# Kernel optimization log

Measured on AMD Instinct MI355X. Metric: run time of the kernel, lower is better.

## Reference

```python
import jax, jax.numpy as jnp
import numpy as np

EPS_ENERGY = 1e-05
EPS_NORM = 1e-05
DN = ('NWC', 'WIO', 'NWC')  # conv1d dimension numbers: (B,L,C) x (K,Cin,Cout)


def setup_inputs() -> dict:
    key = jax.random.key(0)
    k1, k2 = jax.random.split(key)
    B, L, C = 16, 32768, 21
    K, F = 9, 128
    inputs = jax.random.normal(k1, (B, L, C), dtype=jnp.float32)
    kernel = jax.random.normal(k2, (K, C, F), dtype=jnp.float32)
    # UnitNorm constraint over axes [0, 1] (per output filter)
    kernel = kernel / jnp.sqrt(jnp.sum(kernel * kernel, axis=(0, 1), keepdims=True))
    scale = jnp.full((1, 1, 1), 10.0, dtype=jnp.float32)  # initial_scale
    bias = jnp.zeros((F,), dtype=jnp.float32)
    return {"inputs": inputs, "kernel": kernel, "scale": scale, "bias": bias}


def reference(inputs, kernel, scale, bias):
    # dot: (B, L-K+1, F)
    dot = jax.lax.conv_general_dilated(
        inputs, kernel, window_strides=(1,), padding='VALID',
        dimension_numbers=DN)
    # patch energy: sliding sum of squares over window and ALL input channels.
    # Original convolves sq_inputs with an all-ones (K, C, F) kernel, producing
    # the identical value in every filter channel; we compute it once with a
    # (K, C, 1) ones kernel and broadcast -- same math, less traffic.
    K, C, _ = kernel.shape
    ones_k = jnp.ones((K, C, 1), dtype=inputs.dtype)
    patch_energy = jax.lax.conv_general_dilated(
        inputs * inputs, ones_k, window_strides=(1,), padding='VALID',
        dimension_numbers=DN)  # (B, Lout, 1)
    patch_norms = jnp.sqrt(patch_energy + EPS_ENERGY)
    return scale * (dot / (patch_norms + EPS_NORM)) + bias
```

## Files before the change

### kernel.cpp

```cpp
#include <hip/hip_runtime.h>
#include <hip/hip_bf16.h>
#include <math.h>

typedef __bf16 bf16x8 __attribute__((ext_vector_type(8)));
typedef float  f32x4  __attribute__((ext_vector_type(4)));
typedef unsigned short u16x8 __attribute__((ext_vector_type(8)));

#define B_      16
#define LIN_    32768
#define LOUT_   32760
#define CIN_    21
#define CPAD_   24
#define KT_     9
#define F_      128
#define KSTEPS_ 7
#define TILE_L_ 256
#define ROWS_   264
#define ROWSA_  266
#define NTILE_  128
#define OBST_   136

__device__ __forceinline__ unsigned short f2bf(float f) {
  unsigned u = __float_as_uint(f);
  u += 0x7FFFu + ((u >> 16) & 1u);
  return (unsigned short)(u >> 16);
}
__device__ __forceinline__ float bf2f(unsigned short h) {
  return __uint_as_float(((unsigned)h) << 16);
}

__global__ __launch_bounds__(256, 3)
void ckn1d_mfma(const float* __restrict__ X, const float* __restrict__ W,
                const float* __restrict__ scale_p, const float* __restrict__ bias_p,
                float* __restrict__ Y)
{
  __shared__ __align__(16) unsigned short tileA[ROWSA_ * CPAD_];
  __shared__ float rowsq[ROWS_];
  __shared__ float inv_s[TILE_L_];
  __shared__ __align__(16) float outbuf[64 * OBST_];

  const int tid  = threadIdx.x;
  const int wv   = tid >> 6;
  const int lane = tid & 63;
  const int la   = lane & 15;
  const int q    = lane >> 4;

  const int bx   = blockIdx.x;
  const int b    = bx >> 7;
  const int tile = bx & (NTILE_ - 1);
  const int l0t  = tile * TILE_L_;

  const float scale = scale_p[0];
  const int f0 = wv * 32 + la;
  const float bias0 = bias_p[f0];
  const float bias1 = bias_p[f0 + 16];

  u16x8 bw[KSTEPS_][2];
  #pragma unroll
  for (int t = 0; t < KSTEPS_; ++t) {
    #pragma unroll
    for (int nf = 0; nf < 2; ++nf) {
      #pragma unroll
      for (int j = 0; j < 8; ++j) {
        int r = t * 32 + q * 8 + j;
        int k = r / CPAD_;
        int c = r - k * CPAD_;
        float v = 0.f;
        if (c < CIN_ && k < KT_) v = W[(k * CIN_ + c) * F_ + f0 + nf * 16];
        bw[t][nf][j] = f2bf(v);
      }
    }
  }

  const float* __restrict__ Xb = X + (size_t)b * LIN_ * CIN_;
  float*       __restrict__ Yb = Y + (size_t)b * LOUT_ * F_;

  for (int i = tid; i < ROWSA_ * 3; i += 256) {
    int r = i / 3;
    tileA[r * CPAD_ + CIN_ + (i - r * 3)] = 0;
  }
  for (int i = tid; i < 2 * CIN_; i += 256) {
    int r = ROWS_ + i / CIN_;
    tileA[r * CPAD_ + (i % CIN_)] = 0;
  }
  {
    const float* src = Xb + (size_t)l0t * CIN_;
    const int nvalid = min(ROWS_ * CIN_, (LIN_ - l0t) * CIN_);
    const int n4v = nvalid >> 2;
    const float4* src4 = (const float4*)src;
    for (int i4 = tid; i4 < (ROWS_ * CIN_) / 4; i4 += 256) {
      float4 v;
      if (i4 < n4v) v = src4[i4];
      else          v = make_float4(0.f, 0.f, 0.f, 0.f);
      int base = i4 * 4;
      #pragma unroll
      for (int e = 0; e < 4; ++e) {
        int idx = base + e;
        int r = idx / CIN_;
        int c = idx - r * CIN_;
        float x = (e == 0) ? v.x : (e == 1) ? v.y : (e == 2) ? v.z : v.w;
        tileA[r * CPAD_ + c] = f2bf(x);
      }
    }
  }
  __syncthreads();

  for (int r = tid; r < ROWS_; r += 256) {
    const u16x8* rp = (const u16x8*)&tileA[r * CPAD_];
    float s = 0.f;
    #pragma unroll
    for (int g = 0; g < 3; ++g) {
      u16x8 v = rp[g];
      #pragma unroll
      for (int j = 0; j < 8; ++j) { float x = bf2f(v[j]); s += x * x; }
    }
    rowsq[r] = s;
  }
  __syncthreads();

  {
    float e = 0.f;
    #pragma unroll
    for (int t = 0; t < KT_; ++t) e += rowsq[tid + t];
    inv_s[tid] = scale / (sqrtf(e + 1e-5f) + 1e-5f);
  }
  __syncthreads();

  const f32x4 fzero = {0.f, 0.f, 0.f, 0.f};

  for (int sub = 0; sub < 4; ++sub) {
    const int ls = sub * 64;

    f32x4 acc[4][2];
    #pragma unroll
    for (int m = 0; m < 4; ++m) { acc[m][0] = fzero; acc[m][1] = fzero; }

    #pragma unroll
    for (int t = 0; t < KSTEPS_; ++t) {
      #pragma unroll
      for (int m = 0; m < 4; ++m) {
        bf16x8 a = *(const bf16x8*)&tileA[(ls + m * 16 + la) * CPAD_ + t * 32 + q * 8];
        acc[m][0] = __builtin_amdgcn_mfma_f32_16x16x32_bf16(
            a, __builtin_bit_cast(bf16x8, bw[t][0]), acc[m][0], 0, 0, 0);
        acc[m][1] = __builtin_amdgcn_mfma_f32_16x16x32_bf16(
            a, __builtin_bit_cast(bf16x8, bw[t][1]), acc[m][1], 0, 0, 0);
      }
    }

    #pragma unroll
    for (int m = 0; m < 4; ++m) {
      #pragma unroll
      for (int rg = 0; rg < 4; ++rg) {
        int lrow = m * 16 + q * 4 + rg;
        float iv = inv_s[ls + lrow];
        outbuf[lrow * OBST_ + f0]      = acc[m][0][rg] * iv + bias0;
        outbuf[lrow * OBST_ + f0 + 16] = acc[m][1][rg] * iv + bias1;
      }
    }
    __syncthreads();

    {
      const int lg0 = l0t + ls;
      for (int i = tid; i < 64 * 32; i += 256) {
        int r  = i >> 5;
        int c4 = i & 31;
        int lg = lg0 + r;
        if (lg < LOUT_) {
          float4 v = *(const float4*)&outbuf[r * OBST_ + c4 * 4];
          *(float4*)&Yb[(size_t)lg * F_ + c4 * 4] = v;
        }
      }
    }
    __syncthreads();
  }
}

extern "C" void kernel_launch(void* const* d_in, const int* in_sizes, int n_in,
                              void* d_out, int out_size, void* d_ws, size_t ws_size,
                              hipStream_t stream) {
  const float* X  = (const float*)d_in[0];
  const float* W  = (const float*)d_in[1];
  const float* S  = (const float*)d_in[2];
  const float* Bi = (const float*)d_in[3];
  float* Y = (float*)d_out;
  dim3 grid(B_ * NTILE_), block(256);
  ckn1d_mfma<<<grid, block, 0, stream>>>(X, W, S, Bi, Y);
}
```

Before: 83.14 us.

## Store MFMA results directly to global and drop the LDS output staging buffer

Removes the shared-memory output buffer and its two barriers per sub-tile, so each wave writes its MFMA accumulator fragments straight to global memory as scalar 4-byte stores. It also processes one 16-row fragment per loop iteration instead of four, raises the occupancy hint from 3 to 4 blocks, and moves the weight load after the input tile load. Dropping the LDS buffer frees shared memory and barriers, but the global stores become strided 64-byte row segments rather than coalesced float4 rows, which may hurt write efficiency on an output-bandwidth-bound kernel.

After: 88.60 us. 6.6% more time.

```diff
diff --git a/kernel.cpp b/kernel.cpp
--- a/kernel.cpp
+++ b/kernel.cpp
@@ -18,7 +18,6 @@
 #define ROWS_   264
 #define ROWSA_  266
 #define NTILE_  128
-#define OBST_   136
 
 __device__ __forceinline__ unsigned short f2bf(float f) {
   unsigned u = __float_as_uint(f);
@@ -29,15 +28,14 @@
   return __uint_as_float(((unsigned)h) << 16);
 }
 
-__global__ __launch_bounds__(256, 3)
+__global__ __launch_bounds__(256, 4)
 void ckn1d_mfma(const float* __restrict__ X, const float* __restrict__ W,
                 const float* __restrict__ scale_p, const float* __restrict__ bias_p,
                 float* __restrict__ Y)
 {
   __shared__ __align__(16) unsigned short tileA[ROWSA_ * CPAD_];
   __shared__ float rowsq[ROWS_];
-  __shared__ float inv_s[TILE_L_];
-  __shared__ __align__(16) float outbuf[64 * OBST_];
+  __shared__ __align__(16) float inv_s[TILE_L_];
 
   const int tid  = threadIdx.x;
   const int wv   = tid >> 6;
@@ -54,23 +52,6 @@
   const int f0 = wv * 32 + la;
   const float bias0 = bias_p[f0];
   const float bias1 = bias_p[f0 + 16];
-
-  u16x8 bw[KSTEPS_][2];
-  #pragma unroll
-  for (int t = 0; t < KSTEPS_; ++t) {
-    #pragma unroll
-    for (int nf = 0; nf < 2; ++nf) {
-      #pragma unroll
-      for (int j = 0; j < 8; ++j) {
-        int r = t * 32 + q * 8 + j;
-        int k = r / CPAD_;
-        int c = r - k * CPAD_;
-        float v = 0.f;
-        if (c < CIN_ && k < KT_) v = W[(k * CIN_ + c) * F_ + f0 + nf * 16];
-        bw[t][nf][j] = f2bf(v);
-      }
-    }
-  }
 
   const float* __restrict__ Xb = X + (size_t)b * LIN_ * CIN_;
   float*       __restrict__ Yb = Y + (size_t)b * LOUT_ * F_;
@@ -105,6 +86,23 @@
   }
   __syncthreads();
 
+  u16x8 bw[KSTEPS_][2];
+  #pragma unroll
+  for (int t = 0; t < KSTEPS_; ++t) {
+    #pragma unroll
+    for (int nf = 0; nf < 2; ++nf) {
+      #pragma unroll
+      for (int j = 0; j < 8; ++j) {
+        int r = t * 32 + q * 8 + j;
+        int k = r / CPAD_;
+        int c = r - k * CPAD_;
+        float v = 0.f;
+        if (c < CIN_ && k < KT_) v = W[(k * CIN_ + c) * F_ + f0 + nf * 16];
+        bw[t][nf][j] = f2bf(v);
+      }
+    }
+  }
+
   for (int r = tid; r < ROWS_; r += 256) {
     const u16x8* rp = (const u16x8*)&tileA[r * CPAD_];
     float s = 0.f;
@@ -127,51 +125,40 @@
   __syncthreads();
 
   const f32x4 fzero = {0.f, 0.f, 0.f, 0.f};
+  const bool full = (l0t + TILE_L_) <= LOUT_;
 
-  for (int sub = 0; sub < 4; ++sub) {
-    const int ls = sub * 64;
-
-    f32x4 acc[4][2];
-    #pragma unroll
-    for (int m = 0; m < 4; ++m) { acc[m][0] = fzero; acc[m][1] = fzero; }
-
+  #pragma unroll 1
+  for (int mf = 0; mf < 16; ++mf) {
+    const unsigned short* arow = &tileA[(mf * 16 + la) * CPAD_ + q * 8];
+    f32x4 a0 = fzero, a1 = fzero;
     #pragma unroll
     for (int t = 0; t < KSTEPS_; ++t) {
-      #pragma unroll
-      for (int m = 0; m < 4; ++m) {
-        bf16x8 a = *(const bf16x8*)&tileA[(ls + m * 16 + la) * CPAD_ + t * 32 + q * 8];
-        acc[m][0] = __builtin_amdgcn_mfma_f32_16x16x32_bf16(
-            a, __builtin_bit_cast(bf16x8, bw[t][0]), acc[m][0], 0, 0, 0);
-        acc[m][1] = __builtin_amdgcn_mfma_f32_16x16x32_bf16(
-            a, __builtin_bit_cast(bf16x8, bw[t][1]), acc[m][1], 0, 0, 0);
-      }
+      bf16x8 a = *(const bf16x8*)&arow[t * 32];
+      a0 = __builtin_amdgcn_mfma_f32_16x16x32_bf16(
+          a, __builtin_bit_cast(bf16x8, bw[t][0]), a0, 0, 0, 0);
+      a1 = __builtin_amdgcn_mfma_f32_16x16x32_bf16(
+          a, __builtin_bit_cast(bf16x8, bw[t][1]), a1, 0, 0, 0);
     }
-
-    #pragma unroll
-    for (int m = 0; m < 4; ++m) {
+    const int lrow0 = mf * 16 + q * 4;
+    const f32x4 iv4 = *(const f32x4*)&inv_s[lrow0];
+    float* yo = Yb + (size_t)(l0t + lrow0) * F_ + f0;
+    if (full) {
       #pragma unroll
       for (int rg = 0; rg < 4; ++rg) {
-        int lrow = m * 16 + q * 4 + rg;
-        float iv = inv_s[ls + lrow];
-        outbuf[lrow * OBST_ + f0]      = acc[m][0][rg] * iv + bias0;
-        outbuf[lrow * OBST_ + f0 + 16] = acc[m][1][rg] * iv + bias1;
+        float iv = iv4[rg];
+        yo[(size_t)rg * F_]      = a0[rg] * iv + bias0;
+        yo[(size_t)rg * F_ + 16] = a1[rg] * iv + bias1;
       }
-    }
-    __syncthreads();
-
-    {
-      const int lg0 = l0t + ls;
-      for (int i = tid; i < 64 * 32; i += 256) {
-        int r  = i >> 5;
-        int c4 = i & 31;
-        int lg = lg0 + r;
-        if (lg < LOUT_) {
-          float4 v = *(const float4*)&outbuf[r * OBST_ + c4 * 4];
-          *(float4*)&Yb[(size_t)lg * F_ + c4 * 4] = v;
+    } else {
+      #pragma unroll
+      for (int rg = 0; rg < 4; ++rg) {
+        float iv = iv4[rg];
+        if (l0t + lrow0 + rg < LOUT_) {
+          yo[(size_t)rg * F_]      = a0[rg] * iv + bias0;
+          yo[(size_t)rg * F_ + 16] = a1[rg] * iv + bias1;
         }
       }
     }
-    __syncthreads();
   }
 }
 
```
